# Performance work log

Hardware: AMD Instinct MI355X
Metric: run time of the kernel (lower is better)

## Reference

```python
import jax, jax.numpy as jnp
import numpy as np
import math

DIM = 768
NUM_HEADS = 16
PERHEAD = DIM // NUM_HEADS  # 48
B, T = 4, 2048


def setup_inputs() -> dict:
    key = jax.random.key(0)
    k_x, k_wi, k_bi, k_wo, k_bo = jax.random.split(key, 5)
    s_in = 1.0 / math.sqrt(DIM)
    return {
        "x": jax.random.normal(k_x, (B, T, DIM), dtype=jnp.float32),
        # linear_in: y = x @ w_in + b_in, w_in: (DIM, 3*DIM)
        "w_in": jax.random.uniform(k_wi, (DIM, 3 * DIM), jnp.float32, -s_in, s_in),
        "b_in": jax.random.uniform(k_bi, (3 * DIM,), jnp.float32, -s_in, s_in),
        "w_out": jax.random.uniform(k_wo, (DIM, DIM), jnp.float32, -s_in, s_in),
        "b_out": jax.random.uniform(k_bo, (DIM,), jnp.float32, -s_in, s_in),
    }


def reference(x, w_in, b_in, w_out, b_out):
    bs, tok, _ = x.shape
    qkv = x @ w_in + b_in                                   # (B, T, 3*DIM)
    # Faithful to torch: reshape to (B, T, H, 3*ph), move heads, chunk last dim.
    qkv = qkv.reshape(bs, tok, NUM_HEADS, 3 * PERHEAD)
    qkv = jnp.transpose(qkv, (0, 2, 1, 3))                  # (B, H, T, 3*ph)
    q, k, v = jnp.split(qkv, 3, axis=-1)                    # each (B, H, T, ph)
    scale = 1.0 / math.sqrt(PERHEAD)
    scores = jnp.einsum("bhqd,bhkd->bhqk", q, k) * scale    # (B, H, T, T)
    attn = jax.nn.softmax(scores, axis=-1)
    # dropout p=0.0 (eval) -> identity
    out = jnp.einsum("bhqk,bhkd->bhqd", attn, v)            # (B, H, T, ph)
    out = jnp.transpose(out, (0, 2, 1, 3)).reshape(bs, tok, DIM)
    return out @ w_out + b_out
```

## Files before the change

### kernel.cpp

```cpp
#include <hip/hip_runtime.h>
#include <hip/hip_bf16.h>
#include <math.h>

typedef __attribute__((ext_vector_type(8))) short short8;
typedef __attribute__((ext_vector_type(4))) float floatx4;
typedef __hip_bfloat16 bf16;

#define DIM 768
#define NHEADS 16
#define PH 48
#define VROWS 49
#define BATCH 4
#define SEQ 2048
#define MTOK (BATCH*SEQ)
#define NQKV (3*DIM)
#define NQK (2*DIM)
#define LOG2E 1.44269504088896f
#define CFAC (0.14433756729740643f * LOG2E)

#define NB_CAST   6144
#define NB_TWIN   1728
#define NB_TWOUT  576
#define NB_MISC   140

__device__ __forceinline__ void cp16(void* dst, const void* src) {
    *(float4*)dst = *(const float4*)src;
}
__device__ __forceinline__ unsigned short f2us(float v) {
    bf16 b = __float2bfloat16(v);
    return *(unsigned short*)&b;
}
__device__ __forceinline__ float us2f(unsigned short u) {
    bf16 b = *(bf16*)&u;
    return __bfloat162float(b);
}
__device__ __forceinline__ void gload_lds16(const bf16* g, bf16* l) {
    __builtin_amdgcn_global_load_lds(
        (const __attribute__((address_space(1))) unsigned int*)g,
        (__attribute__((address_space(3))) unsigned int*)l, 16, 0, 0);
}
__device__ __forceinline__ bool sniff_f32(const unsigned short* __restrict__ x) {
    float v = us2f(x[threadIdx.x & 63]);
    int bad = !(fabsf(v) < 64.0f);
    return __any(bad) != 0;
}

__global__ __launch_bounds__(256) void prep_all(
    const void* __restrict__ x, const void* __restrict__ w_in,
    const void* __restrict__ w_out, const void* __restrict__ bin,
    const void* __restrict__ bout,
    bf16* __restrict__ xb, bf16* __restrict__ winT, bf16* __restrict__ woutT,
    float* __restrict__ bi, float* __restrict__ bo, bf16* __restrict__ Vt)
{
    __shared__ bf16 tile[32][33];
    const int bid = blockIdx.x, tid = threadIdx.x;
    const bool f32 = sniff_f32((const unsigned short*)x);

    if (bid < NB_CAST) {
        int i = bid * 256 + tid;
        if (f32) {
            float4 v = ((const float4*)x)[i];
            ushort4 o;
            o.x = f2us(v.x); o.y = f2us(v.y); o.z = f2us(v.z); o.w = f2us(v.w);
            ((ushort4*)xb)[i] = o;
        } else {
            ((ushort4*)xb)[i] = ((const ushort4*)x)[i];
        }
    } else if (bid < NB_CAST + NB_TWIN + NB_TWOUT) {
        const void* in; bf16* out; int R, C, tt;
        if (bid < NB_CAST + NB_TWIN) {
            in = w_in; out = winT; R = DIM; C = NQKV; tt = bid - NB_CAST;
        } else {
            in = w_out; out = woutT; R = DIM; C = DIM; tt = bid - NB_CAST - NB_TWIN;
        }
        int ctiles = C / 32;
        int c0 = (tt % ctiles) * 32, r0 = (tt / ctiles) * 32;
        int tx = tid & 31, ty = tid >> 5;
#pragma unroll
        for (int j = 0; j < 4; j++) {
            size_t idx = (size_t)(r0 + ty + 8*j) * C + c0 + tx;
            float v = f32 ? ((const float*)in)[idx]
                          : us2f(((const unsigned short*)in)[idx]);
            tile[ty + 8*j][tx] = __float2bfloat16(v);
        }
        __syncthreads();
#pragma unroll
        for (int j = 0; j < 4; j++)
            out[(size_t)(c0 + ty + 8*j) * R + r0 + tx] = tile[tx][ty + 8*j];
    } else {
        int t = (bid - (NB_CAST + NB_TWIN + NB_TWOUT)) * 256 + tid;
        if (t < NQKV) {
            bi[t] = f32 ? ((const float*)bin)[t] : us2f(((const unsigned short*)bin)[t]);
        } else if (t < NQKV + DIM) {
            int j = t - NQKV;
            bo[j] = f32 ? ((const float*)bout)[j] : us2f(((const unsigned short*)bout)[j]);
        } else {
            int k = t - (NQKV + DIM);
            int bh = k >> 9, pos = (k & 511) * 4;
            bf16* dst = Vt + ((size_t)bh * VROWS + 48) * SEQ + pos;
            ushort4 ones;
            ones.x = ones.y = ones.z = ones.w = f2us(1.0f);
            *(ushort4*)dst = ones;
        }
    }
}

template<int N, int MODE>
__global__ __launch_bounds__(256) void gemm_bias(
    const bf16* __restrict__ A, const bf16* __restrict__ BT,
    const float* __restrict__ bias, void* __restrict__ C0, bf16* __restrict__ Vt,
    const unsigned short* __restrict__ xraw)
{
    constexpr int K = 768;
    __shared__ __align__(16) bf16 smem[2 * 128 * 32];
    bf16* As = smem;
    bf16* Bs = smem + 128 * 32;
    const bool out_f32 = (MODE == 2) && sniff_f32(xraw);
    const int tid = threadIdx.x;
    const int id = blockIdx.x;
    const int m0 = (id & 63) * 128, n0 = (id >> 6) * 128;
    const int w = tid >> 6, lane = tid & 63, lq = lane >> 4, ln = lane & 15;
    const int wr = w & 1, wc = w >> 1;

    const int rl0 = w * 32 + (lane >> 2);
    const int rl1 = rl0 + 16;
    const int ssw = ((lane >> 2) ^ (lane >> 4)) & 3;
    const int cm = (lane & 3) ^ ssw;
    const bf16* gA0 = A + (size_t)(m0 + rl0) * K + cm * 8;
    const bf16* gA1 = A + (size_t)(m0 + rl1) * K + cm * 8;
    const bf16* gB0 = BT + (size_t)(n0 + rl0) * K + cm * 8;
    const bf16* gB1 = BT + (size_t)(n0 + rl1) * K + cm * 8;
    bf16* lA0 = &As[(w * 32 + 0) * 32];
    bf16* lA1 = &As[(w * 32 + 16) * 32];
    bf16* lB0 = &Bs[(w * 32 + 0) * 32];
    bf16* lB1 = &Bs[(w * 32 + 16) * 32];

    const int rsw = (ln ^ (ln >> 2)) & 3;
    const int rchunk = (lq ^ rsw) * 8;

    floatx4 zero4 = {0.f, 0.f, 0.f, 0.f};
    floatx4 acc[4][4];
#pragma unroll
    for (int mi = 0; mi < 4; mi++)
#pragma unroll
        for (int nj = 0; nj < 4; nj++) acc[mi][nj] = zero4;

    for (int k0 = 0; k0 < K; k0 += 32) {
        gload_lds16(gA0, lA0);
        gload_lds16(gA1, lA1);
        gload_lds16(gB0, lB0);
        gload_lds16(gB1, lB1);
        gA0 += 32; gA1 += 32; gB0 += 32; gB1 += 32;
        __syncthreads();

        short8 a[4], b[4];
#pragma unroll
        for (int mi = 0; mi < 4; mi++)
            a[mi] = *(const short8*)&As[(wr * 64 + 16 * mi + ln) * 32 + rchunk];
#pragma unroll
        for (int nj = 0; nj < 4; nj++)
            b[nj] = *(const short8*)&Bs[(wc * 64 + 16 * nj + ln) * 32 + rchunk];
#pragma unroll
        for (int mi = 0; mi < 4; mi++)
#pragma unroll
            for (int nj = 0; nj < 4; nj++)
                acc[mi][nj] = __builtin_amdgcn_mfma_f32_16x16x32_bf16(
                    a[mi], b[nj], acc[mi][nj], 0, 0, 0);
        __syncthreads();
    }
    bf16 (*VLs)[136] = (bf16(*)[136])smem;

#pragma unroll
    for (int nj = 0; nj < 4; nj++) {
        int n = n0 + wc * 64 + 16 * nj + ln;
        float bv = bias[n];
        if (MODE == 2) {
#pragma unroll
            for (int mi = 0; mi < 4; mi++)
#pragma unroll
                for (int i = 0; i < 4; i++) {
                    size_t off = (size_t)(m0 + wr * 64 + 16 * mi + 4 * lq + i) * N + n;
                    float val = acc[mi][nj][i] + bv;
                    if (out_f32) ((float*)C0)[off] = val;
                    else         ((bf16*)C0)[off] = __float2bfloat16(val);
                }
        } else {
            int h = n / 144, r = n - 144 * h;
            if (r < 96) {
                float sc = (r < 48) ? CFAC : 1.0f;
#pragma unroll
                for (int mi = 0; mi < 4; mi++)
#pragma unroll
                    for (int i = 0; i < 4; i++) {
                        size_t off = (size_t)(m0 + wr * 64 + 16 * mi + 4 * lq + i) * NQK
                                     + h * 96 + r;
                        ((bf16*)C0)[off] = __float2bfloat16((acc[mi][nj][i] + bv) * sc);
                    }
            } else {
                int d = r - 96;
#pragma unroll
                for (int mi = 0; mi < 4; mi++)
#pragma unroll
                    for (int i = 0; i < 4; i++)
                        VLs[d][wr * 64 + 16 * lq + 4 * i + mi] =
                            __float2bfloat16(acc[mi][nj][i] + bv);
            }
        }
    }

    if (MODE == 1) {
        __syncthreads();
        const int bidx = m0 >> 11, tok0 = m0 & 2047;
#pragma unroll
        for (int s = 0; s < 3; s++) {
            int idx = tid + 256 * s;
            int d = idx >> 4, ch = idx & 15;
            int h = (n0 + 31 - d) / 144;
            int n = 144 * h + 96 + d;
            if (n >= n0 && n < n0 + 128) {
                bf16* dst = Vt + ((size_t)(bidx * NHEADS + h) * VROWS + d) * SEQ
                            + tok0 + ch * 8;
                *(float4*)dst = *(const float4*)&VLs[d][ch * 8];
            }
        }
    }
}

__global__ __launch_bounds__(256, 2) void attn_fused(
    const bf16* __restrict__ QK, const bf16* __restrict__ Vt, bf16* __restrict__ O)
{
    __shared__ bf16 QPs[256][72];
    __shared__ bf16 Ks[64][72];
    __shared__ bf16 VsT[64][72];

    const int tid = threadIdx.x;
    const int id = blockIdx.x;
    const int g = id & 63, qt = id >> 6;
    const int h = g & 15, b = g >> 4;
    const int w = tid >> 6, lane = tid & 63, lq = lane >> 4, ln = lane & 15;
    const size_t rowbase = (size_t)b * SEQ;
    const int q0 = qt * 256;
    const int hoff = h * 96;
    const bf16* Vth = Vt + (size_t)(b * NHEADS + h) * VROWS * SEQ;

    const bf16 bzero = __float2bfloat16(0.f);
    for (int idx = tid; idx < 4096; idx += 256)
        QPs[idx >> 4][48 + (idx & 15)] = bzero;
    for (int idx = tid; idx < 1024; idx += 256)
        Ks[idx >> 4][48 + (idx & 15)] = bzero;

#pragma unroll
    for (int s = 0; s < 6; s++) {
        int idx = tid + 256 * s, r = idx / 6, c = idx % 6;
        cp16(&QPs[r][c * 8], &QK[(rowbase + q0 + r) * NQK + hoff + c * 8]);
    }
    __syncthreads();

    short8 qa0[4], qa1[4];
#pragma unroll
    for (int f = 0; f < 4; f++) {
        qa0[f] = *(const short8*)&QPs[64*f + 16*w + ln][lq * 8];
        qa1[f] = *(const short8*)&QPs[64*f + 16*w + ln][lq * 8 + 32];
    }

    const int kr0a = tid / 6, kc0a = tid % 6;
    const int kr1a = (tid + 256) / 6, kc1a = (tid + 256) % 6;
    const char* kg0 = (const char*)(QK + (rowbase + kr0a) * NQK + hoff + 48) + kc0a * 16;
    const char* kg1 = (const char*)(QK + (rowbase + kr1a) * NQK + hoff + 48) + kc1a * 16;
    bf16* kd0 = &Ks[kr0a][kc0a * 8];
    bf16* kd1 = &Ks[kr1a][kc1a * 8];
    const bool kact = (tid < 128);
    const int vr0 = tid >> 3, vc0 = tid & 7;
    const char* vg0 = (const char*)(Vth + (size_t)vr0 * SEQ) + vc0 * 16;
    const char* vg1 = (const char*)(Vth + (size_t)(32 + vr0) * SEQ) + vc0 * 16;
    bf16* vd0 = &VsT[vr0][vc0 * 8];
    bf16* vd1 = &VsT[32 + vr0][vc0 * 8];
    const bool vact = (tid < 136);
    const ptrdiff_t KADV = (ptrdiff_t)64 * NQK * 2;
    const ptrdiff_t VADV = 128;

    floatx4 zero4 = {0.f, 0.f, 0.f, 0.f};
    floatx4 o[4][4];
#pragma unroll
    for (int f = 0; f < 4; f++)
#pragma unroll
        for (int nt = 0; nt < 4; nt++) o[f][nt] = zero4;

    float4 rk0, rk1, rv0, rv1;
    rk0 = *(const float4*)kg0;
    if (kact) rk1 = *(const float4*)kg1;
    rv0 = *(const float4*)vg0;
    if (vact) rv1 = *(const float4*)vg1;
    kg0 += KADV; kg1 += KADV; vg0 += VADV; vg1 += VADV;

    for (int kt = 0; kt < 32; kt++) {
        __syncthreads();
        *(float4*)kd0 = rk0;
        if (kact) *(float4*)kd1 = rk1;
        *(float4*)vd0 = rv0;
        if (vact) *(float4*)vd1 = rv1;
        if (kt < 31) {
            rk0 = *(const float4*)kg0;
            if (kact) rk1 = *(const float4*)kg1;
            rv0 = *(const float4*)vg0;
            if (vact) rv1 = *(const float4*)vg1;
            kg0 += KADV; kg1 += KADV; vg0 += VADV; vg1 += VADV;
        }
        __syncthreads();

        short8 kb0[4], kb1[4];
#pragma unroll
        for (int t = 0; t < 4; t++) {
            kb0[t] = *(const short8*)&Ks[16*t + ln][lq * 8];
            kb1[t] = *(const short8*)&Ks[16*t + ln][lq * 8 + 32];
        }

#pragma unroll
        for (int f = 0; f < 4; f++) {
            floatx4 s[4];
#pragma unroll
            for (int t = 0; t < 4; t++) s[t] = zero4;
#pragma unroll
            for (int t = 0; t < 4; t++) {
                s[t] = __builtin_amdgcn_mfma_f32_16x16x32_bf16(qa0[f], kb0[t], s[t], 0, 0, 0);
                s[t] = __builtin_amdgcn_mfma_f32_16x16x32_bf16(qa1[f], kb1[t], s[t], 0, 0, 0);
            }
#pragma unroll
            for (int i = 0; i < 4; i++) {
                union { ushort4 u4; __hip_bfloat162 h2[2]; } pk;
                float2 p01, p23;
                p01.x = __builtin_amdgcn_exp2f(s[0][i]);
                p01.y = __builtin_amdgcn_exp2f(s[1][i]);
                p23.x = __builtin_amdgcn_exp2f(s[2][i]);
                p23.y = __builtin_amdgcn_exp2f(s[3][i]);
                pk.h2[0] = __float22bfloat162_rn(p01);
                pk.h2[1] = __float22bfloat162_rn(p23);
                *(ushort4*)&QPs[64*f + 16*w + 4*lq + i][4*ln] = pk.u4;
            }
        }

#pragma unroll
        for (int ks = 0; ks < 2; ks++) {
            short8 pa[4];
#pragma unroll
            for (int f = 0; f < 4; f++)
                pa[f] = *(const short8*)&QPs[64*f + 16*w + ln][lq * 8 + 32*ks];
#pragma unroll
            for (int nt = 0; nt < 4; nt++) {
                short8 vb = *(const short8*)&VsT[16*nt + ln][lq * 8 + 32*ks];
#pragma unroll
                for (int f = 0; f < 4; f++)
                    o[f][nt] = __builtin_amdgcn_mfma_f32_16x16x32_bf16(pa[f], vb, o[f][nt], 0, 0, 0);
            }
        }
    }

#pragma unroll
    for (int f = 0; f < 4; f++)
#pragma unroll
        for (int i = 0; i < 4; i++) {
            float l = __shfl(o[f][3][i], (lane >> 4) << 4);
            float inv = 1.0f / l;
            int row = q0 + 64*f + 16*w + 4*lq + i;
#pragma unroll
            for (int nt = 0; nt < 3; nt++)
                O[(rowbase + row) * DIM + h * PH + 16*nt + ln] =
                    __float2bfloat16(o[f][nt][i] * inv);
        }
}

extern "C" void kernel_launch(void* const* d_in, const int* in_sizes, int n_in,
                              void* d_out, int out_size, void* d_ws, size_t ws_size,
                              hipStream_t stream) {
    const void* x     = d_in[0];
    const void* w_in  = d_in[1];
    const void* b_in  = d_in[2];
    const void* w_out = d_in[3];
    const void* b_out = d_in[4];

    bf16* qk    = (bf16*)d_ws;
    bf16* Vt    = qk    + (size_t)MTOK * NQK;
    bf16* xb    = Vt    + (size_t)BATCH * NHEADS * VROWS * SEQ;
    bf16* attn  = xb;
    bf16* winT  = xb    + (size_t)MTOK * DIM;
    bf16* woutT = winT  + (size_t)NQKV * DIM;
    float* bi   = (float*)(woutT + (size_t)DIM * DIM);
    float* bo   = bi + NQKV;

    prep_all<<<NB_CAST + NB_TWIN + NB_TWOUT + NB_MISC, 256, 0, stream>>>(
        x, w_in, w_out, b_in, b_out, xb, winT, woutT, bi, bo, Vt);

    gemm_bias<NQKV, 1><<<64 * (NQKV/128), 256, 0, stream>>>(
        xb, winT, bi, qk, Vt, (const unsigned short*)x);
    attn_fused<<<64 * (SEQ/256), 256, 0, stream>>>(qk, Vt, attn);
    gemm_bias<DIM, 2><<<64 * (DIM/128), 256, 0, stream>>>(
        attn, woutT, bo, d_out, nullptr, (const unsigned short*)x);
}
```

Measured before the change: 230.8 us.

## Keep P in registers via transposed QK^T MFMA and double-buffer K/V tiles

The score MFMA now takes swapped operands (K as A, Q as B), so each lane's exponentiated scores already match the A-operand layout for the PV MFMA. This removes the P round-trip through shared memory, and the V staging layout in the projection kernel is permuted to match. Q is loaded straight from global into registers, the QPs shared buffer is dropped, and K/V tiles are double-buffered so each iteration needs one barrier instead of two. s_setprio is raised around the compute section to favour MFMA issue; the cost is more register pressure from holding pa[4][2] and a permuted key order that must line up exactly with the V layout.

Result: faster. 212.4 us (-8.0%).

```diff
diff --git a/kernel.cpp b/kernel.cpp
--- a/kernel.cpp
+++ b/kernel.cpp
@@ -202,7 +202,7 @@
                 for (int mi = 0; mi < 4; mi++)
 #pragma unroll
                     for (int i = 0; i < 4; i++)
-                        VLs[d][wr * 64 + 16 * lq + 4 * i + mi] =
+                        VLs[d][wr * 64 + 32 * (mi >> 1) + 8 * lq + 4 * (mi & 1) + i] =
                             __float2bfloat16(acc[mi][nj][i] + bv);
             }
         }
@@ -229,9 +229,8 @@
 __global__ __launch_bounds__(256, 2) void attn_fused(
     const bf16* __restrict__ QK, const bf16* __restrict__ Vt, bf16* __restrict__ O)
 {
-    __shared__ bf16 QPs[256][72];
-    __shared__ bf16 Ks[64][72];
-    __shared__ bf16 VsT[64][72];
+    __shared__ bf16 Ks[2][64][72];
+    __shared__ bf16 VsT[2][64][72];
 
     const int tid = threadIdx.x;
     const int id = blockIdx.x;
@@ -244,40 +243,36 @@
     const bf16* Vth = Vt + (size_t)(b * NHEADS + h) * VROWS * SEQ;
 
     const bf16 bzero = __float2bfloat16(0.f);
-    for (int idx = tid; idx < 4096; idx += 256)
-        QPs[idx >> 4][48 + (idx & 15)] = bzero;
-    for (int idx = tid; idx < 1024; idx += 256)
-        Ks[idx >> 4][48 + (idx & 15)] = bzero;
-
-#pragma unroll
-    for (int s = 0; s < 6; s++) {
-        int idx = tid + 256 * s, r = idx / 6, c = idx % 6;
-        cp16(&QPs[r][c * 8], &QK[(rowbase + q0 + r) * NQK + hoff + c * 8]);
-    }
-    __syncthreads();
+    for (int idx = tid; idx < 2048; idx += 256) {
+        int bb = idx >> 10, r = (idx >> 4) & 63, c = idx & 15;
+        Ks[bb][r][48 + c] = bzero;
+    }
 
     short8 qa0[4], qa1[4];
+    short8 zero8 = {0, 0, 0, 0, 0, 0, 0, 0};
 #pragma unroll
     for (int f = 0; f < 4; f++) {
-        qa0[f] = *(const short8*)&QPs[64*f + 16*w + ln][lq * 8];
-        qa1[f] = *(const short8*)&QPs[64*f + 16*w + ln][lq * 8 + 32];
+        const bf16* qrow = QK + (rowbase + q0 + 64*f + 16*w + ln) * NQK + hoff;
+        qa0[f] = *(const short8*)(qrow + lq * 8);
+        qa1[f] = (lq < 2) ? *(const short8*)(qrow + 32 + lq * 8) : zero8;
     }
 
     const int kr0a = tid / 6, kc0a = tid % 6;
     const int kr1a = (tid + 256) / 6, kc1a = (tid + 256) % 6;
     const char* kg0 = (const char*)(QK + (rowbase + kr0a) * NQK + hoff + 48) + kc0a * 16;
     const char* kg1 = (const char*)(QK + (rowbase + kr1a) * NQK + hoff + 48) + kc1a * 16;
-    bf16* kd0 = &Ks[kr0a][kc0a * 8];
-    bf16* kd1 = &Ks[kr1a][kc1a * 8];
+    bf16* kd0 = &Ks[0][kr0a][kc0a * 8];
+    bf16* kd1 = &Ks[0][kr1a & 63][kc1a * 8];
     const bool kact = (tid < 128);
     const int vr0 = tid >> 3, vc0 = tid & 7;
     const char* vg0 = (const char*)(Vth + (size_t)vr0 * SEQ) + vc0 * 16;
     const char* vg1 = (const char*)(Vth + (size_t)(32 + vr0) * SEQ) + vc0 * 16;
-    bf16* vd0 = &VsT[vr0][vc0 * 8];
-    bf16* vd1 = &VsT[32 + vr0][vc0 * 8];
+    bf16* vd0 = &VsT[0][vr0][vc0 * 8];
+    bf16* vd1 = &VsT[0][32 + vr0][vc0 * 8];
     const bool vact = (tid < 136);
     const ptrdiff_t KADV = (ptrdiff_t)64 * NQK * 2;
     const ptrdiff_t VADV = 128;
+    const int BOFF = 64 * 72;
 
     floatx4 zero4 = {0.f, 0.f, 0.f, 0.f};
     floatx4 o[4][4];
@@ -292,29 +287,46 @@
     rv0 = *(const float4*)vg0;
     if (vact) rv1 = *(const float4*)vg1;
     kg0 += KADV; kg1 += KADV; vg0 += VADV; vg1 += VADV;
+    *(float4*)kd0 = rk0;
+    if (kact) *(float4*)kd1 = rk1;
+    *(float4*)vd0 = rv0;
+    if (vact) *(float4*)vd1 = rv1;
+    rk0 = *(const float4*)kg0;
+    if (kact) rk1 = *(const float4*)kg1;
+    rv0 = *(const float4*)vg0;
+    if (vact) rv1 = *(const float4*)vg1;
+    kg0 += KADV; kg1 += KADV; vg0 += VADV; vg1 += VADV;
+    __syncthreads();
 
     for (int kt = 0; kt < 32; kt++) {
-        __syncthreads();
-        *(float4*)kd0 = rk0;
-        if (kact) *(float4*)kd1 = rk1;
-        *(float4*)vd0 = rv0;
-        if (vact) *(float4*)vd1 = rv1;
+        const int cur = kt & 1;
         if (kt < 31) {
-            rk0 = *(const float4*)kg0;
-            if (kact) rk1 = *(const float4*)kg1;
-            rv0 = *(const float4*)vg0;
-            if (vact) rv1 = *(const float4*)vg1;
-            kg0 += KADV; kg1 += KADV; vg0 += VADV; vg1 += VADV;
-        }
-        __syncthreads();
-
+            const int nb = (cur ^ 1) * BOFF;
+            *(float4*)(kd0 + nb) = rk0;
+            if (kact) *(float4*)(kd1 + nb) = rk1;
+            *(float4*)(vd0 + nb) = rv0;
+            if (vact) *(float4*)(vd1 + nb) = rv1;
+            if (kt < 30) {
+                rk0 = *(const float4*)kg0;
+                if (kact) rk1 = *(const float4*)kg1;
+                rv0 = *(const float4*)vg0;
+                if (vact) rv1 = *(const float4*)vg1;
+                kg0 += KADV; kg1 += KADV; vg0 += VADV; vg1 += VADV;
+            }
+        }
+
+        const bf16 (*Kc)[72] = Ks[cur];
+        const bf16 (*Vc)[72] = VsT[cur];
+
+        __builtin_amdgcn_s_setprio(1);
         short8 kb0[4], kb1[4];
 #pragma unroll
         for (int t = 0; t < 4; t++) {
-            kb0[t] = *(const short8*)&Ks[16*t + ln][lq * 8];
-            kb1[t] = *(const short8*)&Ks[16*t + ln][lq * 8 + 32];
-        }
-
+            kb0[t] = *(const short8*)&Kc[16*t + ln][lq * 8];
+            kb1[t] = *(const short8*)&Kc[16*t + ln][lq * 8 + 32];
+        }
+
+        short8 pa[4][2];
 #pragma unroll
         for (int f = 0; f < 4; f++) {
             floatx4 s[4];
@@ -322,37 +334,41 @@
             for (int t = 0; t < 4; t++) s[t] = zero4;
 #pragma unroll
             for (int t = 0; t < 4; t++) {
-                s[t] = __builtin_amdgcn_mfma_f32_16x16x32_bf16(qa0[f], kb0[t], s[t], 0, 0, 0);
-                s[t] = __builtin_amdgcn_mfma_f32_16x16x32_bf16(qa1[f], kb1[t], s[t], 0, 0, 0);
-            }
-#pragma unroll
-            for (int i = 0; i < 4; i++) {
-                union { ushort4 u4; __hip_bfloat162 h2[2]; } pk;
-                float2 p01, p23;
-                p01.x = __builtin_amdgcn_exp2f(s[0][i]);
-                p01.y = __builtin_amdgcn_exp2f(s[1][i]);
-                p23.x = __builtin_amdgcn_exp2f(s[2][i]);
-                p23.y = __builtin_amdgcn_exp2f(s[3][i]);
-                pk.h2[0] = __float22bfloat162_rn(p01);
-                pk.h2[1] = __float22bfloat162_rn(p23);
-                *(ushort4*)&QPs[64*f + 16*w + 4*lq + i][4*ln] = pk.u4;
-            }
-        }
-
-#pragma unroll
-        for (int ks = 0; ks < 2; ks++) {
-            short8 pa[4];
-#pragma unroll
-            for (int f = 0; f < 4; f++)
-                pa[f] = *(const short8*)&QPs[64*f + 16*w + ln][lq * 8 + 32*ks];
-#pragma unroll
-            for (int nt = 0; nt < 4; nt++) {
-                short8 vb = *(const short8*)&VsT[16*nt + ln][lq * 8 + 32*ks];
-#pragma unroll
-                for (int f = 0; f < 4; f++)
-                    o[f][nt] = __builtin_amdgcn_mfma_f32_16x16x32_bf16(pa[f], vb, o[f][nt], 0, 0, 0);
-            }
-        }
+                s[t] = __builtin_amdgcn_mfma_f32_16x16x32_bf16(kb0[t], qa0[f], s[t], 0, 0, 0);
+                s[t] = __builtin_amdgcn_mfma_f32_16x16x32_bf16(kb1[t], qa1[f], s[t], 0, 0, 0);
+            }
+#pragma unroll
+            for (int ks = 0; ks < 2; ks++) {
+                union { short8 v; __hip_bfloat162 h2[4]; } u;
+                float2 p;
+                p.x = __builtin_amdgcn_exp2f(s[2*ks][0]);
+                p.y = __builtin_amdgcn_exp2f(s[2*ks][1]);
+                u.h2[0] = __float22bfloat162_rn(p);
+                p.x = __builtin_amdgcn_exp2f(s[2*ks][2]);
+                p.y = __builtin_amdgcn_exp2f(s[2*ks][3]);
+                u.h2[1] = __float22bfloat162_rn(p);
+                p.x = __builtin_amdgcn_exp2f(s[2*ks+1][0]);
+                p.y = __builtin_amdgcn_exp2f(s[2*ks+1][1]);
+                u.h2[2] = __float22bfloat162_rn(p);
+                p.x = __builtin_amdgcn_exp2f(s[2*ks+1][2]);
+                p.y = __builtin_amdgcn_exp2f(s[2*ks+1][3]);
+                u.h2[3] = __float22bfloat162_rn(p);
+                pa[f][ks] = u.v;
+            }
+        }
+
+#pragma unroll
+        for (int nt = 0; nt < 4; nt++) {
+            short8 vb0 = *(const short8*)&Vc[16*nt + ln][lq * 8];
+            short8 vb1 = *(const short8*)&Vc[16*nt + ln][lq * 8 + 32];
+#pragma unroll
+            for (int f = 0; f < 4; f++) {
+                o[f][nt] = __builtin_amdgcn_mfma_f32_16x16x32_bf16(pa[f][0], vb0, o[f][nt], 0, 0, 0);
+                o[f][nt] = __builtin_amdgcn_mfma_f32_16x16x32_bf16(pa[f][1], vb1, o[f][nt], 0, 0, 0);
+            }
+        }
+        __builtin_amdgcn_s_setprio(0);
+        __syncthreads();
     }
 
 #pragma unroll
```
